# Optimization experiments

Hardware: AMD Instinct MI355X
Metric: run time of the kernel (lower is better)

Reference implementation:

```python
import jax, jax.numpy as jnp
import numpy as np

B, L, D, H, FF = 8, 512, 1024, 16, 1024
HD = D // H
EPS = 1e-5
ROPE_BASE = 10000.0
ROPE_DIM = D  # module passes dim=embed_dim (not head_dim) to RotaryPositionalEmbeddings


def _layer_norm(x, g, b):
    m = jnp.mean(x, axis=-1, keepdims=True)
    v = jnp.var(x, axis=-1, keepdims=True)
    return (x - m) * jax.lax.rsqrt(v + EPS) * g + b


def _rope(x):
    # x: [B, H, L, HD]; interleaved-pair rotation, frequencies base**(-2i/ROPE_DIM)
    half = HD // 2
    inv_freq = 1.0 / (ROPE_BASE ** (jnp.arange(half, dtype=jnp.float32) * 2.0 / ROPE_DIM))
    ang = jnp.arange(L, dtype=jnp.float32)[:, None] * inv_freq[None, :]  # [L, half]
    cos = jnp.cos(ang)
    sin = jnp.sin(ang)
    xr = x.reshape(*x.shape[:-1], half, 2)
    x1, x2 = xr[..., 0], xr[..., 1]
    out = jnp.stack([x1 * cos - x2 * sin, x1 * sin + x2 * cos], axis=-1)
    return out.reshape(x.shape).astype(x.dtype)


def setup_inputs() -> dict:
    key = jax.random.key(0)
    ks = jax.random.split(key, 16)
    sd = 0.02
    n = lambda k, shape: (jax.random.normal(k, shape, dtype=jnp.float32) * sd)
    return {
        "input_ids": jax.random.normal(ks[0], (B, L, D), dtype=jnp.float32),
        "Wq": n(ks[1], (FF, D)), "bq": jnp.zeros((D,), jnp.float32),
        "Wk": n(ks[2], (FF, D)), "bk": jnp.zeros((D,), jnp.float32),
        "Wv": n(ks[3], (FF, D)), "bv": jnp.zeros((D,), jnp.float32),
        "Wo": n(ks[4], (D, D)),  "bo": jnp.zeros((D,), jnp.float32),
        "Wf": n(ks[5], (D, FF)), "bf": jnp.zeros((FF,), jnp.float32),
        "g_ffn": jnp.ones((D,), jnp.float32), "b_ffn": jnp.zeros((D,), jnp.float32),
        "g_attn": jnp.ones((FF,), jnp.float32), "b_attn": jnp.zeros((FF,), jnp.float32),
    }


def reference(input_ids, Wq, bq, Wk, bk, Wv, bv, Wo, bo, Wf, bf,
              g_ffn, b_ffn, g_attn, b_attn):
    # FFN branch: computed then DISCARDED in the original source (x is overwritten).
    _ffn_dead = jax.nn.relu(_layer_norm(input_ids, g_ffn, b_ffn) @ Wf + bf)  # noqa: F841

    x = _layer_norm(input_ids, g_attn, b_attn)  # pre_attn_norm applied to input_ids
    q = (x @ Wq + bq).reshape(B, L, H, HD).transpose(0, 2, 1, 3)  # [B,H,L,HD]
    k = (x @ Wk + bk).reshape(B, L, H, HD).transpose(0, 2, 1, 3)
    v = (x @ Wv + bv).reshape(B, L, H, HD).transpose(0, 2, 1, 3)
    q = _rope(q)
    k = _rope(k)

    scale = 1.0 / np.sqrt(HD).astype(np.float32)
    scores = jnp.einsum("bhqd,bhkd->bhqk", q, k) * scale  # [B,H,L,L]
    attn = jax.nn.softmax(scores, axis=-1)
    o = jnp.einsum("bhqk,bhkd->bhqd", attn, v)
    o = o.transpose(0, 2, 1, 3).reshape(B, L, D)
    return input_ids + (o @ Wo + bo)
```

## Files before the change

### kernel.cpp

```cpp
#include <hip/hip_runtime.h>

typedef unsigned short ushort_t;
typedef short bf16x8 __attribute__((ext_vector_type(8)));
typedef float f32x4 __attribute__((ext_vector_type(4)));

#define B_ 8
#define L_ 512
#define D_ 1024
#define H_ 16
#define M_ 4096

__device__ __forceinline__ ushort_t f2bf(float f) {
  union { float f; unsigned u; } v; v.f = f;
  unsigned r = v.u + 0x7FFFu + ((v.u >> 16) & 1u);
  return (ushort_t)(r >> 16);
}

__device__ __forceinline__ void gl_lds16(const ushort_t* g, ushort_t* s) {
  __builtin_amdgcn_global_load_lds((const __attribute__((address_space(1))) void*)(g),
                                   (__attribute__((address_space(3))) void*)(s), 16, 0, 0);
}

__global__ __launch_bounds__(256) void prep_kernel(const float* __restrict__ x,
                                                   const float* __restrict__ g,
                                                   const float* __restrict__ b,
                                                   ushort_t* __restrict__ xn,
                                                   float2* __restrict__ csb,
                                                   const float* __restrict__ w0,
                                                   const float* __restrict__ w1,
                                                   const float* __restrict__ w2,
                                                   const float* __restrict__ w3,
                                                   ushort_t* __restrict__ wt) {
  __shared__ float red[8];
  __shared__ float tile[32][33];
  int blk = blockIdx.x, t = threadIdx.x;
  if (blk < 4096) {
    int row = blk;
    float4 v = ((const float4*)(x + (size_t)row * D_))[t];
    float s  = v.x + v.y + v.z + v.w;
    float s2 = v.x * v.x + v.y * v.y + v.z * v.z + v.w * v.w;
#pragma unroll
    for (int m = 1; m < 64; m <<= 1) { s += __shfl_xor(s, m); s2 += __shfl_xor(s2, m); }
    int w = t >> 6;
    if ((t & 63) == 0) { red[w] = s; red[4 + w] = s2; }
    __syncthreads();
    s  = red[0] + red[1] + red[2] + red[3];
    s2 = red[4] + red[5] + red[6] + red[7];
    float mean = s * (1.0f / D_);
    float var  = s2 * (1.0f / D_) - mean * mean;
    float rs   = rsqrtf(var + 1e-5f);
    float4 gg = ((const float4*)g)[t];
    float4 bb = ((const float4*)b)[t];
    unsigned long long pk =
        (unsigned long long)f2bf((v.x - mean) * rs * gg.x + bb.x)
      | ((unsigned long long)f2bf((v.y - mean) * rs * gg.y + bb.y) << 16)
      | ((unsigned long long)f2bf((v.z - mean) * rs * gg.z + bb.z) << 32)
      | ((unsigned long long)f2bf((v.w - mean) * rs * gg.w + bb.w) << 48);
    *(unsigned long long*)(xn + (size_t)row * D_ + t * 4) = pk;
  } else if (blk < 4160) {
    int idx = (blk - 4096) * 256 + t;
    int l = idx >> 5, i = idx & 31;
    float inv = powf(10000.0f, (-2.0f * (float)i) / 1024.0f);
    float ang = (float)l * inv;
    csb[idx] = make_float2(cosf(ang), sinf(ang));
  } else {
    int wb = blk - 4160;
    int z = wb >> 10;
    const float* W = (z == 0) ? w0 : (z == 1) ? w1 : (z == 2) ? w2 : w3;
    ushort_t* WT = wt + ((size_t)z << 20);
    int rem = wb & 1023;
    int by = rem >> 5, bx = rem & 31;
    int tx = t & 31, ty = t >> 5;
    int k0 = by * 32, n0 = bx * 32;
#pragma unroll
    for (int j = 0; j < 4; ++j)
      tile[ty + 8 * j][tx] = W[(size_t)(k0 + ty + 8 * j) * 1024 + n0 + tx];
    __syncthreads();
#pragma unroll
    for (int j = 0; j < 4; ++j)
      WT[(size_t)(n0 + ty + 8 * j) * 1024 + k0 + tx] = f2bf(tile[tx][ty + 8 * j]);
  }
}

__global__ __launch_bounds__(256) void gemm_qkv_kernel(const ushort_t* __restrict__ xn,
                                                       const ushort_t* __restrict__ wt,
                                                       const float* __restrict__ bq,
                                                       const float* __restrict__ bk,
                                                       const float* __restrict__ bv,
                                                       ushort_t* __restrict__ qb,
                                                       ushort_t* __restrict__ kb,
                                                       ushort_t* __restrict__ vt,
                                                       const float2* __restrict__ csb) {
  __shared__ ushort_t As[128 * 64];
  __shared__ ushort_t Bs[128 * 64];
  int t = threadIdx.x, l = t & 63, w = t >> 6, lr = l & 15, lg = l >> 4;
  int hid = blockIdx.x;
  int lid = (hid & 7) * 96 + (hid >> 3);
  int bx = lid % 24, by = lid / 24;
  int m0 = by * 128;
  int n0g = bx * 128;
  int z = n0g >> 10;
  int n0 = n0g & 1023;
  const float* bias = (z == 0) ? bq : (z == 1) ? bk : bv;
  int wr = w >> 1, wc = w & 1;
  const int srow = l >> 3;
  const int scol = ((l & 7) ^ (srow & 7)) * 8;

  f32x4 acc[4][4] = {};

  for (int k0 = 0; k0 < 1024; k0 += 64) {
#pragma unroll
    for (int i = 0; i < 4; ++i) {
      gl_lds16(&xn[(size_t)(m0 + w * 32 + i * 8 + srow) * 1024 + k0 + scol],
               &As[(w * 32 + i * 8) * 64]);
      gl_lds16(&wt[(size_t)(n0g + w * 32 + i * 8 + srow) * 1024 + k0 + scol],
               &Bs[(w * 32 + i * 8) * 64]);
    }
    __syncthreads();
#pragma unroll
    for (int kk = 0; kk < 2; ++kk) {
      bf16x8 a[4], bfr[4];
#pragma unroll
      for (int mi = 0; mi < 4; ++mi)
        a[mi] = *(const bf16x8*)&As[(wr * 64 + mi * 16 + lr) * 64 + (((kk * 4 + lg) ^ (lr & 7)) << 3)];
#pragma unroll
      for (int ni = 0; ni < 4; ++ni)
        bfr[ni] = *(const bf16x8*)&Bs[(wc * 64 + ni * 16 + lr) * 64 + (((kk * 4 + lg) ^ (lr & 7)) << 3)];
#pragma unroll
      for (int mi = 0; mi < 4; ++mi)
#pragma unroll
        for (int ni = 0; ni < 4; ++ni)
          acc[mi][ni] = __builtin_amdgcn_mfma_f32_16x16x32_bf16(a[mi], bfr[ni], acc[mi][ni], 0, 0, 0);
    }
    __syncthreads();
  }

  if (z < 2) {
    ushort_t* outp = (z == 0) ? qb : kb;
    const float sc = (z == 0) ? 0.125f : 1.0f;
#pragma unroll
    for (int mi = 0; mi < 4; ++mi) {
      int rowb = m0 + wr * 64 + mi * 16 + lg * 4;
#pragma unroll
      for (int ni = 0; ni < 4; ++ni) {
        int col = n0 + wc * 64 + ni * 16 + lr;
        float bvv = bias[col];
        int ii = (col & 63) >> 1;
        int codd = col & 1;
#pragma unroll
        for (int r = 0; r < 4; ++r) {
          float val = acc[mi][ni][r] + bvv;
          float par = __shfl_xor(val, 1);
          float2 cs = csb[((rowb + r) & 511) * 32 + ii];
          float y = codd ? (par * cs.y + val * cs.x) : (val * cs.x - par * cs.y);
          outp[(size_t)(rowb + r) * 1024 + col] = f2bf(y * sc);
        }
      }
    }
  } else {
#pragma unroll
    for (int mi = 0; mi < 4; ++mi) {
      int rowb = m0 + wr * 64 + mi * 16 + lg * 4;
      int bidx = rowb >> 9, l0 = rowb & 511;
#pragma unroll
      for (int ni = 0; ni < 4; ++ni) {
        int col = n0 + wc * 64 + ni * 16 + lr;
        float bvv = bias[col];
        unsigned long long pk =
            (unsigned long long)f2bf(acc[mi][ni][0] + bvv)
          | ((unsigned long long)f2bf(acc[mi][ni][1] + bvv) << 16)
          | ((unsigned long long)f2bf(acc[mi][ni][2] + bvv) << 32)
          | ((unsigned long long)f2bf(acc[mi][ni][3] + bvv) << 48);
        *(unsigned long long*)&vt[((size_t)(bidx << 10) + col) * 512 + l0] = pk;
      }
    }
  }
}

__global__ __launch_bounds__(256) void gemm_o_kernel(const ushort_t* __restrict__ A,
                                                     const ushort_t* __restrict__ Bt,
                                                     const float* __restrict__ bias,
                                                     const float* __restrict__ res,
                                                     float* __restrict__ out) {
  __shared__ ushort_t As[64 * 64];
  __shared__ ushort_t Bs[128 * 64];
  int t = threadIdx.x, l = t & 63, w = t >> 6, lr = l & 15, lg = l >> 4;
  int hid = blockIdx.x;
  int lid = (hid & 7) * 64 + (hid >> 3);
  int bx = lid & 7, by = lid >> 3;
  int m0 = by * 64, n0 = bx * 128;
  int wr = w >> 1, wc = w & 1;
  const int srow = l >> 3;
  const int scol = ((l & 7) ^ (srow & 7)) * 8;

  f32x4 acc[2][4] = {};

  for (int k0 = 0; k0 < 1024; k0 += 64) {
#pragma unroll
    for (int i = 0; i < 2; ++i)
      gl_lds16(&A[(size_t)(m0 + w * 16 + i * 8 + srow) * 1024 + k0 + scol],
               &As[(w * 16 + i * 8) * 64]);
#pragma unroll
    for (int i = 0; i < 4; ++i)
      gl_lds16(&Bt[(size_t)(n0 + w * 32 + i * 8 + srow) * 1024 + k0 + scol],
               &Bs[(w * 32 + i * 8) * 64]);
    __syncthreads();
#pragma unroll
    for (int kk = 0; kk < 2; ++kk) {
      bf16x8 a[2], bfr[4];
#pragma unroll
      for (int mi = 0; mi < 2; ++mi)
        a[mi] = *(const bf16x8*)&As[(wr * 32 + mi * 16 + lr) * 64 + (((kk * 4 + lg) ^ (lr & 7)) << 3)];
#pragma unroll
      for (int ni = 0; ni < 4; ++ni)
        bfr[ni] = *(const bf16x8*)&Bs[(wc * 64 + ni * 16 + lr) * 64 + (((kk * 4 + lg) ^ (lr & 7)) << 3)];
#pragma unroll
      for (int mi = 0; mi < 2; ++mi)
#pragma unroll
        for (int ni = 0; ni < 4; ++ni)
          acc[mi][ni] = __builtin_amdgcn_mfma_f32_16x16x32_bf16(a[mi], bfr[ni], acc[mi][ni], 0, 0, 0);
    }
    __syncthreads();
  }

#pragma unroll
  for (int mi = 0; mi < 2; ++mi) {
    int rowb = m0 + wr * 32 + mi * 16 + lg * 4;
#pragma unroll
    for (int ni = 0; ni < 4; ++ni) {
      int col = n0 + wc * 64 + ni * 16 + lr;
      float bvv = bias[col];
#pragma unroll
      for (int r = 0; r < 4; ++r) {
        size_t off = (size_t)(rowb + r) * 1024 + col;
        out[off] = acc[mi][ni][r] + bvv + res[off];
      }
    }
  }
}

__global__ __launch_bounds__(256) void attn_kernel(const ushort_t* __restrict__ q,
                                                   const ushort_t* __restrict__ k,
                                                   const ushort_t* __restrict__ vt,
                                                   ushort_t* __restrict__ o) {
  __shared__ ushort_t Ks[2][64 * 64];
  __shared__ ushort_t Vs[2][64 * 64];
  __shared__ ushort_t Ps[4][4][16 * 64];
  int t = threadIdx.x, l = t & 63, w = t >> 6, lr = l & 15, lg = l >> 4;
  int blk = blockIdx.x;
  int bh = blk & 127, qt = blk >> 7;
  int b = bh >> 4, h = bh & 15;
  const int srow = l >> 3;
  const int scol = ((l & 7) ^ (srow & 7)) * 8;

  bf16x8 qf[4][2];
#pragma unroll
  for (int qm = 0; qm < 4; ++qm) {
    size_t qrow = (size_t)(b * 512 + qt * 256 + w * 64 + qm * 16 + lr);
#pragma unroll
    for (int kh = 0; kh < 2; ++kh)
      qf[qm][kh] = *(const bf16x8*)&q[qrow * 1024 + h * 64 + kh * 32 + lg * 8];
  }

  f32x4 oacc[4][4] = {};
  float mrun[4] = {-1e30f, -1e30f, -1e30f, -1e30f};
  float lrun[4] = {0.f, 0.f, 0.f, 0.f};

#define STAGE(buf, kv0)                                                              \
  {                                                                                  \
    _Pragma("unroll")                                                                \
    for (int j = 0; j < 2; ++j) {                                                    \
      gl_lds16(&k[(size_t)(b * 512 + (kv0) + w * 16 + j * 8 + srow) * 1024 + h * 64 + scol], \
               &Ks[buf][(w * 16 + j * 8) * 64]);                                     \
      gl_lds16(&vt[((size_t)bh * 64 + w * 16 + j * 8 + srow) * 512 + (kv0) + scol],  \
               &Vs[buf][(w * 16 + j * 8) * 64]);                                     \
    }                                                                                \
  }

  STAGE(0, 0);
  __syncthreads();
  int cur = 0;
  for (int it = 0; it < 8; ++it) {
    if (it < 7) { STAGE(cur ^ 1, (it + 1) * 64); }
    bf16x8 kf[2][4];
#pragma unroll
    for (int kh = 0; kh < 2; ++kh)
#pragma unroll
      for (int kn = 0; kn < 4; ++kn)
        kf[kh][kn] = *(const bf16x8*)&Ks[cur][(kn * 16 + lr) * 64 + (((kh * 4 + lg) ^ (lr & 7)) << 3)];

#pragma unroll
    for (int qm = 0; qm < 4; ++qm) {
      f32x4 st[4] = {};
#pragma unroll
      for (int kh = 0; kh < 2; ++kh)
#pragma unroll
        for (int kn = 0; kn < 4; ++kn)
          st[kn] = __builtin_amdgcn_mfma_f32_16x16x32_bf16(kf[kh][kn], qf[qm][kh], st[kn], 0, 0, 0);
      float mx = st[0][0];
#pragma unroll
      for (int kn = 0; kn < 4; ++kn)
#pragma unroll
        for (int r = 0; r < 4; ++r) mx = fmaxf(mx, st[kn][r]);
      mx = fmaxf(mx, __shfl_xor(mx, 16));
      mx = fmaxf(mx, __shfl_xor(mx, 32));
      float mn = mrun[qm], al = 1.0f;
      if (!__all(mx <= mrun[qm] + 8.0f)) {
        mn = fmaxf(mrun[qm], mx);
        al = __expf(mrun[qm] - mn);
        mrun[qm] = mn;
#pragma unroll
        for (int f = 0; f < 4; ++f) {
          oacc[qm][f][0] *= al; oacc[qm][f][1] *= al;
          oacc[qm][f][2] *= al; oacc[qm][f][3] *= al;
        }
      }
      float sm = 0.f;
#pragma unroll
      for (int kn = 0; kn < 4; ++kn) {
        float p0 = __expf(st[kn][0] - mn);
        float p1 = __expf(st[kn][1] - mn);
        float p2 = __expf(st[kn][2] - mn);
        float p3 = __expf(st[kn][3] - mn);
        sm += p0 + p1 + p2 + p3;
        int kvb = kn * 16 + 4 * lg;
        unsigned long long pk =
            (unsigned long long)f2bf(p0)
          | ((unsigned long long)f2bf(p1) << 16)
          | ((unsigned long long)f2bf(p2) << 32)
          | ((unsigned long long)f2bf(p3) << 48);
        *(unsigned long long*)&Ps[w][qm][lr * 64 + (((kvb >> 3) ^ (lr & 7)) << 3) + (kvb & 7)] = pk;
      }
      sm += __shfl_xor(sm, 16);
      sm += __shfl_xor(sm, 32);
      lrun[qm] = lrun[qm] * al + sm;
    }
    asm volatile("s_waitcnt lgkmcnt(0)" ::: "memory");
    __builtin_amdgcn_sched_barrier(0);
#pragma unroll
    for (int kk = 0; kk < 2; ++kk) {
      int sl = (((kk * 4 + lg) ^ (lr & 7)) << 3);
      bf16x8 pb[4];
#pragma unroll
      for (int qm = 0; qm < 4; ++qm)
        pb[qm] = *(const bf16x8*)&Ps[w][qm][lr * 64 + sl];
#pragma unroll
      for (int f = 0; f < 4; ++f) {
        bf16x8 vf = *(const bf16x8*)&Vs[cur][(f * 16 + lr) * 64 + sl];
#pragma unroll
        for (int qm = 0; qm < 4; ++qm)
          oacc[qm][f] = __builtin_amdgcn_mfma_f32_16x16x32_bf16(vf, pb[qm], oacc[qm][f], 0, 0, 0);
      }
    }
    __syncthreads();
    cur ^= 1;
  }
#pragma unroll
  for (int qm = 0; qm < 4; ++qm) {
    float inv = 1.0f / lrun[qm];
    size_t qrow = (size_t)(b * 512 + qt * 256 + w * 64 + qm * 16 + lr);
#pragma unroll
    for (int f = 0; f < 4; ++f) {
      unsigned long long pk =
          (unsigned long long)f2bf(oacc[qm][f][0] * inv)
        | ((unsigned long long)f2bf(oacc[qm][f][1] * inv) << 16)
        | ((unsigned long long)f2bf(oacc[qm][f][2] * inv) << 32)
        | ((unsigned long long)f2bf(oacc[qm][f][3] * inv) << 48);
      *(unsigned long long*)&o[qrow * 1024 + h * 64 + f * 16 + 4 * lg] = pk;
    }
  }
#undef STAGE
}

extern "C" void kernel_launch(void* const* d_in, const int* in_sizes, int n_in,
                              void* d_out, int out_size, void* d_ws, size_t ws_size,
                              hipStream_t stream) {
  const float* input_ids = (const float*)d_in[0];
  const float* Wq = (const float*)d_in[1];
  const float* bq = (const float*)d_in[2];
  const float* Wk = (const float*)d_in[3];
  const float* bk = (const float*)d_in[4];
  const float* Wv = (const float*)d_in[5];
  const float* bv = (const float*)d_in[6];
  const float* Wo = (const float*)d_in[7];
  const float* bo = (const float*)d_in[8];
  const float* g_attn = (const float*)d_in[13];
  const float* b_attn = (const float*)d_in[14];
  float* out = (float*)d_out;

  char* ws = (char*)d_ws;
  const size_t MB = 1024 * 1024;
  ushort_t* wt = (ushort_t*)(ws);
  ushort_t* xn = (ushort_t*)(ws + 8 * MB);
  ushort_t* qb = (ushort_t*)(ws + 16 * MB);
  ushort_t* kb = (ushort_t*)(ws + 24 * MB);
  ushort_t* vt = (ushort_t*)(ws + 32 * MB);
  float2* csb  = (float2*)(ws + 40 * MB);

  prep_kernel<<<8256, 256, 0, stream>>>(input_ids, g_attn, b_attn, xn, csb,
                                        Wq, Wk, Wv, Wo, wt);
  gemm_qkv_kernel<<<768, 256, 0, stream>>>(xn, wt, bq, bk, bv, qb, kb, vt, csb);
  attn_kernel<<<256, 256, 0, stream>>>(qb, kb, vt, xn);
  gemm_o_kernel<<<512, 256, 0, stream>>>(xn, wt + 3 * MB, bo, input_ids, out);
}
```

Baseline: 106.7 us.

## Double-buffer GEMM LDS tiles and halve attention query tile for more blocks

Both GEMM kernels now use two LDS buffers, so the global-to-LDS loads for the next K tile are issued before the MFMA work on the current tile. This replaces the old load-then-sync pattern and lets memory latency overlap with compute. The attention kernel now handles 128 query rows per block instead of 256, with each wave owning two 16-row groups, and the grid grows to 512 blocks to fill more CUs. In exchange, the QKV GEMM's LDS use doubles, which may reduce blocks per CU, and each attention block reloads K and V for fewer queries, so K/V reuse drops.

Measured after the change: 112.5 us. 1.05x slower.

```diff
diff --git a/kernel.cpp b/kernel.cpp
--- a/kernel.cpp
+++ b/kernel.cpp
@@ -91,8 +91,8 @@
                                                        ushort_t* __restrict__ kb,
                                                        ushort_t* __restrict__ vt,
                                                        const float2* __restrict__ csb) {
-  __shared__ ushort_t As[128 * 64];
-  __shared__ ushort_t Bs[128 * 64];
+  __shared__ ushort_t As[2][128 * 64];
+  __shared__ ushort_t Bs[2][128 * 64];
   int t = threadIdx.x, l = t & 63, w = t >> 6, lr = l & 15, lg = l >> 4;
   int hid = blockIdx.x;
   int lid = (hid & 7) * 96 + (hid >> 3);
@@ -106,26 +106,32 @@
   const int srow = l >> 3;
   const int scol = ((l & 7) ^ (srow & 7)) * 8;
 
+#define STG(buf, k0)                                                              \
+  {                                                                               \
+    _Pragma("unroll")                                                             \
+    for (int i = 0; i < 4; ++i) {                                                 \
+      gl_lds16(&xn[(size_t)(m0 + w * 32 + i * 8 + srow) * 1024 + (k0) + scol],    \
+               &As[buf][(w * 32 + i * 8) * 64]);                                  \
+      gl_lds16(&wt[(size_t)(n0g + w * 32 + i * 8 + srow) * 1024 + (k0) + scol],   \
+               &Bs[buf][(w * 32 + i * 8) * 64]);                                  \
+    }                                                                             \
+  }
+
   f32x4 acc[4][4] = {};
-
-  for (int k0 = 0; k0 < 1024; k0 += 64) {
-#pragma unroll
-    for (int i = 0; i < 4; ++i) {
-      gl_lds16(&xn[(size_t)(m0 + w * 32 + i * 8 + srow) * 1024 + k0 + scol],
-               &As[(w * 32 + i * 8) * 64]);
-      gl_lds16(&wt[(size_t)(n0g + w * 32 + i * 8 + srow) * 1024 + k0 + scol],
-               &Bs[(w * 32 + i * 8) * 64]);
-    }
-    __syncthreads();
+  STG(0, 0);
+  __syncthreads();
+  int cur = 0;
+  for (int it = 0; it < 16; ++it) {
+    if (it < 15) STG(cur ^ 1, (it + 1) * 64);
 #pragma unroll
     for (int kk = 0; kk < 2; ++kk) {
       bf16x8 a[4], bfr[4];
 #pragma unroll
       for (int mi = 0; mi < 4; ++mi)
-        a[mi] = *(const bf16x8*)&As[(wr * 64 + mi * 16 + lr) * 64 + (((kk * 4 + lg) ^ (lr & 7)) << 3)];
+        a[mi] = *(const bf16x8*)&As[cur][(wr * 64 + mi * 16 + lr) * 64 + (((kk * 4 + lg) ^ (lr & 7)) << 3)];
 #pragma unroll
       for (int ni = 0; ni < 4; ++ni)
-        bfr[ni] = *(const bf16x8*)&Bs[(wc * 64 + ni * 16 + lr) * 64 + (((kk * 4 + lg) ^ (lr & 7)) << 3)];
+        bfr[ni] = *(const bf16x8*)&Bs[cur][(wc * 64 + ni * 16 + lr) * 64 + (((kk * 4 + lg) ^ (lr & 7)) << 3)];
 #pragma unroll
       for (int mi = 0; mi < 4; ++mi)
 #pragma unroll
@@ -133,7 +139,9 @@
           acc[mi][ni] = __builtin_amdgcn_mfma_f32_16x16x32_bf16(a[mi], bfr[ni], acc[mi][ni], 0, 0, 0);
     }
     __syncthreads();
-  }
+    cur ^= 1;
+  }
+#undef STG
 
   if (z < 2) {
     ushort_t* outp = (z == 0) ? qb : kb;
@@ -182,8 +190,8 @@
                                                      const float* __restrict__ bias,
                                                      const float* __restrict__ res,
                                                      float* __restrict__ out) {
-  __shared__ ushort_t As[64 * 64];
-  __shared__ ushort_t Bs[128 * 64];
+  __shared__ ushort_t As[2][64 * 64];
+  __shared__ ushort_t Bs[2][128 * 64];
   int t = threadIdx.x, l = t & 63, w = t >> 6, lr = l & 15, lg = l >> 4;
   int hid = blockIdx.x;
   int lid = (hid & 7) * 64 + (hid >> 3);
@@ -193,27 +201,33 @@
   const int srow = l >> 3;
   const int scol = ((l & 7) ^ (srow & 7)) * 8;
 
+#define STG(buf, k0)                                                              \
+  {                                                                               \
+    _Pragma("unroll")                                                             \
+    for (int i = 0; i < 2; ++i)                                                   \
+      gl_lds16(&A[(size_t)(m0 + w * 16 + i * 8 + srow) * 1024 + (k0) + scol],     \
+               &As[buf][(w * 16 + i * 8) * 64]);                                  \
+    _Pragma("unroll")                                                             \
+    for (int i = 0; i < 4; ++i)                                                   \
+      gl_lds16(&Bt[(size_t)(n0 + w * 32 + i * 8 + srow) * 1024 + (k0) + scol],    \
+               &Bs[buf][(w * 32 + i * 8) * 64]);                                  \
+  }
+
   f32x4 acc[2][4] = {};
-
-  for (int k0 = 0; k0 < 1024; k0 += 64) {
-#pragma unroll
-    for (int i = 0; i < 2; ++i)
-      gl_lds16(&A[(size_t)(m0 + w * 16 + i * 8 + srow) * 1024 + k0 + scol],
-               &As[(w * 16 + i * 8) * 64]);
-#pragma unroll
-    for (int i = 0; i < 4; ++i)
-      gl_lds16(&Bt[(size_t)(n0 + w * 32 + i * 8 + srow) * 1024 + k0 + scol],
-               &Bs[(w * 32 + i * 8) * 64]);
-    __syncthreads();
+  STG(0, 0);
+  __syncthreads();
+  int cur = 0;
+  for (int it = 0; it < 16; ++it) {
+    if (it < 15) STG(cur ^ 1, (it + 1) * 64);
 #pragma unroll
     for (int kk = 0; kk < 2; ++kk) {
       bf16x8 a[2], bfr[4];
 #pragma unroll
       for (int mi = 0; mi < 2; ++mi)
-        a[mi] = *(const bf16x8*)&As[(wr * 32 + mi * 16 + lr) * 64 + (((kk * 4 + lg) ^ (lr & 7)) << 3)];
+        a[mi] = *(const bf16x8*)&As[cur][(wr * 32 + mi * 16 + lr) * 64 + (((kk * 4 + lg) ^ (lr & 7)) << 3)];
 #pragma unroll
       for (int ni = 0; ni < 4; ++ni)
-        bfr[ni] = *(const bf16x8*)&Bs[(wc * 64 + ni * 16 + lr) * 64 + (((kk * 4 + lg) ^ (lr & 7)) << 3)];
+        bfr[ni] = *(const bf16x8*)&Bs[cur][(wc * 64 + ni * 16 + lr) * 64 + (((kk * 4 + lg) ^ (lr & 7)) << 3)];
 #pragma unroll
       for (int mi = 0; mi < 2; ++mi)
 #pragma unroll
@@ -221,7 +235,9 @@
           acc[mi][ni] = __builtin_amdgcn_mfma_f32_16x16x32_bf16(a[mi], bfr[ni], acc[mi][ni], 0, 0, 0);
     }
     __syncthreads();
-  }
+    cur ^= 1;
+  }
+#undef STG
 
 #pragma unroll
   for (int mi = 0; mi < 2; ++mi) {
@@ -245,7 +261,7 @@
                                                    ushort_t* __restrict__ o) {
   __shared__ ushort_t Ks[2][64 * 64];
   __shared__ ushort_t Vs[2][64 * 64];
-  __shared__ ushort_t Ps[4][4][16 * 64];
+  __shared__ ushort_t Ps[4][2][16 * 64];
   int t = threadIdx.x, l = t & 63, w = t >> 6, lr = l & 15, lg = l >> 4;
   int blk = blockIdx.x;
   int bh = blk & 127, qt = blk >> 7;
@@ -253,18 +269,18 @@
   const int srow = l >> 3;
   const int scol = ((l & 7) ^ (srow & 7)) * 8;
 
-  bf16x8 qf[4][2];
-#pragma unroll
-  for (int qm = 0; qm < 4; ++qm) {
-    size_t qrow = (size_t)(b * 512 + qt * 256 + w * 64 + qm * 16 + lr);
+  bf16x8 qf[2][2];
+#pragma unroll
+  for (int qm = 0; qm < 2; ++qm) {
+    size_t qrow = (size_t)(b * 512 + qt * 128 + w * 32 + qm * 16 + lr);
 #pragma unroll
     for (int kh = 0; kh < 2; ++kh)
       qf[qm][kh] = *(const bf16x8*)&q[qrow * 1024 + h * 64 + kh * 32 + lg * 8];
   }
 
-  f32x4 oacc[4][4] = {};
-  float mrun[4] = {-1e30f, -1e30f, -1e30f, -1e30f};
-  float lrun[4] = {0.f, 0.f, 0.f, 0.f};
+  f32x4 oacc[2][4] = {};
+  float mrun[2] = {-1e30f, -1e30f};
+  float lrun[2] = {0.f, 0.f};
 
 #define STAGE(buf, kv0)                                                              \
   {                                                                                  \
@@ -290,7 +306,7 @@
         kf[kh][kn] = *(const bf16x8*)&Ks[cur][(kn * 16 + lr) * 64 + (((kh * 4 + lg) ^ (lr & 7)) << 3)];
 
 #pragma unroll
-    for (int qm = 0; qm < 4; ++qm) {
+    for (int qm = 0; qm < 2; ++qm) {
       f32x4 st[4] = {};
 #pragma unroll
       for (int kh = 0; kh < 2; ++kh)
@@ -340,15 +356,15 @@
 #pragma unroll
     for (int kk = 0; kk < 2; ++kk) {
       int sl = (((kk * 4 + lg) ^ (lr & 7)) << 3);
-      bf16x8 pb[4];
-#pragma unroll
-      for (int qm = 0; qm < 4; ++qm)
+      bf16x8 pb[2];
+#pragma unroll
+      for (int qm = 0; qm < 2; ++qm)
         pb[qm] = *(const bf16x8*)&Ps[w][qm][lr * 64 + sl];
 #pragma unroll
       for (int f = 0; f < 4; ++f) {
         bf16x8 vf = *(const bf16x8*)&Vs[cur][(f * 16 + lr) * 64 + sl];
 #pragma unroll
-        for (int qm = 0; qm < 4; ++qm)
+        for (int qm = 0; qm < 2; ++qm)
           oacc[qm][f] = __builtin_amdgcn_mfma_f32_16x16x32_bf16(vf, pb[qm], oacc[qm][f], 0, 0, 0);
       }
     }
@@ -356,9 +372,9 @@
     cur ^= 1;
   }
 #pragma unroll
-  for (int qm = 0; qm < 4; ++qm) {
+  for (int qm = 0; qm < 2; ++qm) {
     float inv = 1.0f / lrun[qm];
-    size_t qrow = (size_t)(b * 512 + qt * 256 + w * 64 + qm * 16 + lr);
+    size_t qrow = (size_t)(b * 512 + qt * 128 + w * 32 + qm * 16 + lr);
 #pragma unroll
     for (int f = 0; f < 4; ++f) {
       unsigned long long pk =
@@ -400,6 +416,6 @@
   prep_kernel<<<8256, 256, 0, stream>>>(input_ids, g_attn, b_attn, xn, csb,
                                         Wq, Wk, Wv, Wo, wt);
   gemm_qkv_kernel<<<768, 256, 0, stream>>>(xn, wt, bq, bk, bv, qb, kb, vt, csb);
-  attn_kernel<<<256, 256, 0, stream>>>(qb, kb, vt, xn);
+  attn_kernel<<<512, 256, 0, stream>>>(qb, kb, vt, xn);
   gemm_o_kernel<<<512, 256, 0, stream>>>(xn, wt + 3 * MB, bo, input_ids, out);
 }
```

## Enlarge QKV GEMM tiles with double-buffered LDS and halve attention query tile

Applied to the files above, without the earlier changes.

The QKV projection GEMM now uses 256x256 tiles with 512 threads (8 waves), double-buffered LDS, and prefetch loads spread across the MFMA sub-steps, raising MFMA priority with setprio. The goal is more data reuse per load and overlap of global-to-LDS copies with compute. The grid drops to 192 blocks, fewer than the CU count on MI355X, so some CUs sit idle. Separately, the attention kernel now handles 128 queries per block instead of 256, doubling the grid to 512 blocks for better CU occupancy at the cost of reloading K/V more often.

Result: faster. 97.29 us (-8.9%).

```diff
diff --git a/kernel.cpp b/kernel.cpp
--- a/kernel.cpp
+++ b/kernel.cpp
@@ -82,65 +82,90 @@
   }
 }
 
-__global__ __launch_bounds__(256) void gemm_qkv_kernel(const ushort_t* __restrict__ xn,
-                                                       const ushort_t* __restrict__ wt,
-                                                       const float* __restrict__ bq,
-                                                       const float* __restrict__ bk,
-                                                       const float* __restrict__ bv,
-                                                       ushort_t* __restrict__ qb,
-                                                       ushort_t* __restrict__ kb,
-                                                       ushort_t* __restrict__ vt,
-                                                       const float2* __restrict__ csb) {
-  __shared__ ushort_t As[128 * 64];
-  __shared__ ushort_t Bs[128 * 64];
+__global__ __launch_bounds__(512, 2) void gemm_qkv_kernel(const ushort_t* __restrict__ xn,
+                                                          const ushort_t* __restrict__ wt,
+                                                          const float* __restrict__ bq,
+                                                          const float* __restrict__ bk,
+                                                          const float* __restrict__ bv,
+                                                          ushort_t* __restrict__ qb,
+                                                          ushort_t* __restrict__ kb,
+                                                          ushort_t* __restrict__ vt,
+                                                          const float2* __restrict__ csb) {
+  __shared__ ushort_t As[2][256 * 64];
+  __shared__ ushort_t Bs[2][256 * 64];
   int t = threadIdx.x, l = t & 63, w = t >> 6, lr = l & 15, lg = l >> 4;
   int hid = blockIdx.x;
-  int lid = (hid & 7) * 96 + (hid >> 3);
-  int bx = lid % 24, by = lid / 24;
-  int m0 = by * 128;
-  int n0g = bx * 128;
+  int lid = (hid & 7) * 24 + (hid >> 3);
+  int by = lid / 12, bx = lid % 12;
+  int m0 = by * 256;
+  int n0g = bx * 256;
   int z = n0g >> 10;
   int n0 = n0g & 1023;
   const float* bias = (z == 0) ? bq : (z == 1) ? bk : bv;
-  int wr = w >> 1, wc = w & 1;
-  const int srow = l >> 3;
-  const int scol = ((l & 7) ^ (srow & 7)) * 8;
-
-  f32x4 acc[4][4] = {};
-
-  for (int k0 = 0; k0 < 1024; k0 += 64) {
-#pragma unroll
-    for (int i = 0; i < 4; ++i) {
-      gl_lds16(&xn[(size_t)(m0 + w * 32 + i * 8 + srow) * 1024 + k0 + scol],
-               &As[(w * 32 + i * 8) * 64]);
-      gl_lds16(&wt[(size_t)(n0g + w * 32 + i * 8 + srow) * 1024 + k0 + scol],
-               &Bs[(w * 32 + i * 8) * 64]);
-    }
-    __syncthreads();
-#pragma unroll
-    for (int kk = 0; kk < 2; ++kk) {
-      bf16x8 a[4], bfr[4];
+  int wr = w >> 2, wc = w & 3;
+  const int sr8 = l >> 3;
+  const int scol = ((l & 7) ^ sr8) * 8;
+
+#define STGA(buf, rb, k0)                                                           \
+  gl_lds16(&xn[(size_t)(m0 + (rb) + w * 8 + sr8) * 1024 + (k0) + scol],             \
+           &As[buf][((rb) + w * 8) * 64]);
+#define STGB(buf, rb, k0)                                                           \
+  gl_lds16(&wt[(size_t)(n0g + (rb) + w * 8 + sr8) * 1024 + (k0) + scol],            \
+           &Bs[buf][((rb) + w * 8) * 64]);
+
+  f32x4 acc[8][4] = {};
+
+  STGA(0, 0, 0) STGA(0, 64, 0) STGA(0, 128, 0) STGA(0, 192, 0)
+  STGB(0, 0, 0) STGB(0, 64, 0) STGB(0, 128, 0) STGB(0, 192, 0)
+  asm volatile("s_waitcnt vmcnt(0)" ::: "memory");
+  __builtin_amdgcn_s_barrier();
+
+  for (int j = 0; j < 16; ++j) {
+    int cur = j & 1, nxt = cur ^ 1, kn = (j + 1) * 64;
+#pragma unroll
+    for (int q = 0; q < 4; ++q) {
+      const int mh = q >> 1, nh = q & 1;
+      bf16x8 a[4][2], bb[2][2];
 #pragma unroll
       for (int mi = 0; mi < 4; ++mi)
-        a[mi] = *(const bf16x8*)&As[(wr * 64 + mi * 16 + lr) * 64 + (((kk * 4 + lg) ^ (lr & 7)) << 3)];
-#pragma unroll
-      for (int ni = 0; ni < 4; ++ni)
-        bfr[ni] = *(const bf16x8*)&Bs[(wc * 64 + ni * 16 + lr) * 64 + (((kk * 4 + lg) ^ (lr & 7)) << 3)];
-#pragma unroll
-      for (int mi = 0; mi < 4; ++mi)
-#pragma unroll
-        for (int ni = 0; ni < 4; ++ni)
-          acc[mi][ni] = __builtin_amdgcn_mfma_f32_16x16x32_bf16(a[mi], bfr[ni], acc[mi][ni], 0, 0, 0);
-    }
-    __syncthreads();
-  }
+#pragma unroll
+        for (int kk = 0; kk < 2; ++kk)
+          a[mi][kk] = *(const bf16x8*)&As[cur][(wr * 128 + (mh * 4 + mi) * 16 + lr) * 64 +
+                                              (((kk * 4 + lg) ^ (lr & 7)) << 3)];
+#pragma unroll
+      for (int ni = 0; ni < 2; ++ni)
+#pragma unroll
+        for (int kk = 0; kk < 2; ++kk)
+          bb[ni][kk] = *(const bf16x8*)&Bs[cur][(wc * 64 + (nh * 2 + ni) * 16 + lr) * 64 +
+                                               (((kk * 4 + lg) ^ (lr & 7)) << 3)];
+      if (j < 15) {
+        if (q == 0) { STGA(nxt, 0, kn) STGA(nxt, 64, kn) STGA(nxt, 128, kn) STGA(nxt, 192, kn) }
+        else if (q == 1) { STGB(nxt, 0, kn) STGB(nxt, 64, kn) STGB(nxt, 128, kn) STGB(nxt, 192, kn) }
+      }
+      __builtin_amdgcn_s_barrier();
+      __builtin_amdgcn_s_setprio(1);
+#pragma unroll
+      for (int kk = 0; kk < 2; ++kk)
+#pragma unroll
+        for (int mi = 0; mi < 4; ++mi)
+#pragma unroll
+          for (int ni = 0; ni < 2; ++ni)
+            acc[mh * 4 + mi][nh * 2 + ni] = __builtin_amdgcn_mfma_f32_16x16x32_bf16(
+                a[mi][kk], bb[ni][kk], acc[mh * 4 + mi][nh * 2 + ni], 0, 0, 0);
+      __builtin_amdgcn_s_setprio(0);
+      if (q == 3 && j < 15) asm volatile("s_waitcnt vmcnt(0)" ::: "memory");
+      __builtin_amdgcn_s_barrier();
+    }
+  }
+#undef STGA
+#undef STGB
 
   if (z < 2) {
     ushort_t* outp = (z == 0) ? qb : kb;
     const float sc = (z == 0) ? 0.125f : 1.0f;
 #pragma unroll
-    for (int mi = 0; mi < 4; ++mi) {
-      int rowb = m0 + wr * 64 + mi * 16 + lg * 4;
+    for (int mi = 0; mi < 8; ++mi) {
+      int rowb = m0 + wr * 128 + mi * 16 + lg * 4;
 #pragma unroll
       for (int ni = 0; ni < 4; ++ni) {
         int col = n0 + wc * 64 + ni * 16 + lr;
@@ -159,8 +184,8 @@
     }
   } else {
 #pragma unroll
-    for (int mi = 0; mi < 4; ++mi) {
-      int rowb = m0 + wr * 64 + mi * 16 + lg * 4;
+    for (int mi = 0; mi < 8; ++mi) {
+      int rowb = m0 + wr * 128 + mi * 16 + lg * 4;
       int bidx = rowb >> 9, l0 = rowb & 511;
 #pragma unroll
       for (int ni = 0; ni < 4; ++ni) {
@@ -245,7 +270,7 @@
                                                    ushort_t* __restrict__ o) {
   __shared__ ushort_t Ks[2][64 * 64];
   __shared__ ushort_t Vs[2][64 * 64];
-  __shared__ ushort_t Ps[4][4][16 * 64];
+  __shared__ ushort_t Ps[4][2][16 * 64];
   int t = threadIdx.x, l = t & 63, w = t >> 6, lr = l & 15, lg = l >> 4;
   int blk = blockIdx.x;
   int bh = blk & 127, qt = blk >> 7;
@@ -253,18 +278,18 @@
   const int srow = l >> 3;
   const int scol = ((l & 7) ^ (srow & 7)) * 8;
 
-  bf16x8 qf[4][2];
-#pragma unroll
-  for (int qm = 0; qm < 4; ++qm) {
-    size_t qrow = (size_t)(b * 512 + qt * 256 + w * 64 + qm * 16 + lr);
+  bf16x8 qf[2][2];
+#pragma unroll
+  for (int qm = 0; qm < 2; ++qm) {
+    size_t qrow = (size_t)(b * 512 + qt * 128 + w * 32 + qm * 16 + lr);
 #pragma unroll
     for (int kh = 0; kh < 2; ++kh)
       qf[qm][kh] = *(const bf16x8*)&q[qrow * 1024 + h * 64 + kh * 32 + lg * 8];
   }
 
-  f32x4 oacc[4][4] = {};
-  float mrun[4] = {-1e30f, -1e30f, -1e30f, -1e30f};
-  float lrun[4] = {0.f, 0.f, 0.f, 0.f};
+  f32x4 oacc[2][4] = {};
+  float mrun[2] = {-1e30f, -1e30f};
+  float lrun[2] = {0.f, 0.f};
 
 #define STAGE(buf, kv0)                                                              \
   {                                                                                  \
@@ -290,7 +315,7 @@
         kf[kh][kn] = *(const bf16x8*)&Ks[cur][(kn * 16 + lr) * 64 + (((kh * 4 + lg) ^ (lr & 7)) << 3)];
 
 #pragma unroll
-    for (int qm = 0; qm < 4; ++qm) {
+    for (int qm = 0; qm < 2; ++qm) {
       f32x4 st[4] = {};
 #pragma unroll
       for (int kh = 0; kh < 2; ++kh)
@@ -340,15 +365,15 @@
 #pragma unroll
     for (int kk = 0; kk < 2; ++kk) {
       int sl = (((kk * 4 + lg) ^ (lr & 7)) << 3);
-      bf16x8 pb[4];
-#pragma unroll
-      for (int qm = 0; qm < 4; ++qm)
+      bf16x8 pb[2];
+#pragma unroll
+      for (int qm = 0; qm < 2; ++qm)
         pb[qm] = *(const bf16x8*)&Ps[w][qm][lr * 64 + sl];
 #pragma unroll
       for (int f = 0; f < 4; ++f) {
         bf16x8 vf = *(const bf16x8*)&Vs[cur][(f * 16 + lr) * 64 + sl];
 #pragma unroll
-        for (int qm = 0; qm < 4; ++qm)
+        for (int qm = 0; qm < 2; ++qm)
           oacc[qm][f] = __builtin_amdgcn_mfma_f32_16x16x32_bf16(vf, pb[qm], oacc[qm][f], 0, 0, 0);
       }
     }
@@ -356,9 +381,9 @@
     cur ^= 1;
   }
 #pragma unroll
-  for (int qm = 0; qm < 4; ++qm) {
+  for (int qm = 0; qm < 2; ++qm) {
     float inv = 1.0f / lrun[qm];
-    size_t qrow = (size_t)(b * 512 + qt * 256 + w * 64 + qm * 16 + lr);
+    size_t qrow = (size_t)(b * 512 + qt * 128 + w * 32 + qm * 16 + lr);
 #pragma unroll
     for (int f = 0; f < 4; ++f) {
       unsigned long long pk =
@@ -399,7 +424,7 @@
 
   prep_kernel<<<8256, 256, 0, stream>>>(input_ids, g_attn, b_attn, xn, csb,
                                         Wq, Wk, Wv, Wo, wt);
-  gemm_qkv_kernel<<<768, 256, 0, stream>>>(xn, wt, bq, bk, bv, qb, kb, vt, csb);
-  attn_kernel<<<256, 256, 0, stream>>>(qb, kb, vt, xn);
+  gemm_qkv_kernel<<<192, 512, 0, stream>>>(xn, wt, bq, bk, bv, qb, kb, vt, csb);
+  attn_kernel<<<512, 256, 0, stream>>>(qb, kb, vt, xn);
   gemm_o_kernel<<<512, 256, 0, stream>>>(xn, wt + 3 * MB, bo, input_ids, out);
 }
```
